# Optimization experiments

Hardware: AMD Instinct MI355X
Metric: run time of the kernel (lower is better)

The kernel has to match this reference:

```python
import jax, jax.numpy as jnp
import numpy as np

N = 25000      # nodes
E = 400000     # edges (before self-loops)
D = 64         # input node feature dim
H = 4          # attention heads
C = 64         # out channels per head (concat=False -> head mean)
L = 3          # stacked layers
NEG_SLOPE = 0.2
EPS = 1e-5


def setup_inputs() -> dict:
    key = jax.random.key(0)
    ks = jax.random.split(key, 8)
    s = 0.1
    return {
        "x": jax.random.normal(ks[0], (N, D), jnp.float32),
        "edge_index": jax.random.randint(ks[1], (2, E), 0, N, dtype=jnp.int64),
        "Wl": jax.random.normal(ks[2], (L, H * C, D), jnp.float32) * s,
        "bl": jnp.zeros((L, H * C), jnp.float32),
        "Wr": jax.random.normal(ks[3], (L, H * C, D), jnp.float32) * s,
        "br": jnp.zeros((L, H * C), jnp.float32),
        "att": jax.random.normal(ks[4], (L, H, C), jnp.float32) * s,
        "conv_bias": jnp.zeros((L, C), jnp.float32),
        "gn_weight": jnp.ones((L, C), jnp.float32),
        "gn_scale": jnp.ones((L, C), jnp.float32),   # GraphNorm mean_scale (alpha)
        "gn_bias": jnp.zeros((L, C), jnp.float32),
    }


def _gat_forward(x, src, dst, Wl, bl, Wr, br, att, conv_bias,
                 gn_weight, gn_scale, gn_bias):
    n = x.shape[0]
    for i in range(L):
        # GATv2Conv (edge_attr=None, concat=False): separate source/target projections
        xl = (x @ Wl[i].T + bl[i]).reshape(n, H, C)  # [N,H,C]
        xr = (x @ Wr[i].T + br[i]).reshape(n, H, C)
        # per-edge attention logits: att . leaky_relu(xl[j] + xr[i])
        e = jax.nn.leaky_relu(xl[src] + xr[dst], NEG_SLOPE)      # [E',H,C]
        logits = jnp.einsum('ehc,hc->eh', e, att[i])             # [E',H]
        # segment softmax over incoming edges of each target node
        m = jax.ops.segment_max(logits, dst, num_segments=n)     # [N,H]
        a = jnp.exp(logits - m[dst])
        denom = jax.ops.segment_sum(a, dst, num_segments=n)      # [N,H]
        alpha = a / denom[dst]                                   # [E',H]
        # weighted scatter-add of source messages, mean over heads
        agg = jax.ops.segment_sum(xl[src] * alpha[:, :, None], dst,
                                  num_segments=n)                # [N,H,C]
        h = agg.mean(axis=1) + conv_bias[i]                      # [N,C]
        # GraphNorm (single graph): x - alpha*mean, scale by rstd
        mu = h.mean(axis=0)
        hc = h - gn_scale[i] * mu
        var = jnp.mean(hc * hc, axis=0)
        x = hc * jax.lax.rsqrt(var + EPS) * gn_weight[i] + gn_bias[i]
        # Dropout p=0 at eval -> identity
    return x


def reference(x, edge_index, Wl, bl, Wr, br, att, conv_bias,
              gn_weight, gn_scale, gn_bias):
    n = x.shape[0]
    loop = jnp.arange(n, dtype=edge_index.dtype)
    # PyG GATv2Conv adds self-loops by default
    src = jnp.concatenate([edge_index[0], loop])
    dst = jnp.concatenate([edge_index[1], loop])
    return _gat_forward(x, src, dst, Wl, bl, Wr, br, att, conv_bias,
                        gn_weight, gn_scale, gn_bias)
```

## Files before the change

### kernel.cpp

```cpp
#include <hip/hip_runtime.h>
#include <hip/hip_fp16.h>
#include <math.h>

#define HC   256
#define DD   64
#define CC   64
#define NLAY 3

#define RCAP    64
#define RCAP_SH 6

typedef _Float16 h2 __attribute__((ext_vector_type(2)));
typedef _Float16 h4 __attribute__((ext_vector_type(4)));
typedef _Float16 h8 __attribute__((ext_vector_type(8)));
typedef float    f4 __attribute__((ext_vector_type(4)));
typedef float    f2 __attribute__((ext_vector_type(2)));

#define XSTR 72

__global__ __launch_bounds__(256) void zero_kernel(int* __restrict__ counts,
                                                   float* __restrict__ stats,
                                                   int n) {
    int i = blockIdx.x * 256 + threadIdx.x;
    if (i < n) counts[i] = 0;
    if (i < NLAY * 128) stats[i] = 0.f;
}

__global__ __launch_bounds__(256) void fill_kernel(const int* __restrict__ srcArr,
                                                   const int* __restrict__ dstArr,
                                                   int* __restrict__ counts,
                                                   int* __restrict__ csr_src,
                                                   int e, int n) {
    int i = blockIdx.x * 256 + threadIdx.x;
    if (i >= e + n) return;
    int s, d;
    if (i < e) { s = srcArr[i]; d = dstArr[i]; }
    else       { s = d = i - e; }
    int slot = atomicAdd(&counts[d], 1);
    if (slot < RCAP) csr_src[(d << RCAP_SH) + slot] = s;
}

__global__ __launch_bounds__(256) void proj_kernel(const float* __restrict__ x,
                                                   const float* __restrict__ Wl,
                                                   const float* __restrict__ bl,
                                                   const float* __restrict__ Wr,
                                                   const float* __restrict__ br,
                                                   __half* __restrict__ xl,
                                                   __half* __restrict__ xr, int n,
                                                   const float* __restrict__ stats,
                                                   const float* __restrict__ pgw,
                                                   const float* __restrict__ pgs,
                                                   const float* __restrict__ pgb) {
    __shared__ _Float16 xs[64 * XSTR];
    __shared__ _Float16 ws[256 * XSTR];
    __shared__ float nrm_a[64], nrm_b[64];
    const int t  = threadIdx.x;
    const int n0 = blockIdx.x * 64;
    const float* Wsel = blockIdx.y ? Wr : Wl;
    const float* bsel = blockIdx.y ? br : bl;
    __half*      osel = blockIdx.y ? xr : xl;

    if (t < 64) {
        float a = 1.f, b = 0.f;
        if (stats) {
            float inv_n = 1.0f / (float)n;
            float mu  = stats[t] * inv_n;
            float eh2 = stats[64 + t] * inv_n;
            float al  = pgs[t];
            float var = eh2 - 2.f * al * mu * mu + al * al * mu * mu;
            float rstd = rsqrtf(var + 1e-5f);
            a = pgw[t] * rstd;
            b = pgb[t] - al * mu * a;
        }
        nrm_a[t] = a; nrm_b[t] = b;
    }
    __syncthreads();

    {
        const float* xb = x + (size_t)n0 * DD;
        const int limit = (n - n0) * DD;
        #pragma unroll
        for (int it = 0; it < 4; ++it) {
            int f = (it * 256 + t) * 4;
            float4 v = make_float4(0.f, 0.f, 0.f, 0.f);
            if (f + 3 < limit) v = *(const float4*)(xb + f);
            else {
                float tmp[4] = {0.f, 0.f, 0.f, 0.f};
                for (int q = 0; q < 4; ++q) if (f + q < limit) tmp[q] = xb[f + q];
                v = make_float4(tmp[0], tmp[1], tmp[2], tmp[3]);
            }
            int d = f & 63;
            const float4 a4 = *(const float4*)&nrm_a[d];
            const float4 b4 = *(const float4*)&nrm_b[d];
            h4 hv;
            hv.x = (_Float16)fmaf(v.x, a4.x, b4.x);
            hv.y = (_Float16)fmaf(v.y, a4.y, b4.y);
            hv.z = (_Float16)fmaf(v.z, a4.z, b4.z);
            hv.w = (_Float16)fmaf(v.w, a4.w, b4.w);
            *(h4*)&xs[(f >> 6) * XSTR + d] = hv;
        }
    }
    {
        #pragma unroll
        for (int it = 0; it < 16; ++it) {
            int f = (it * 256 + t) * 4;
            float4 v = *(const float4*)(Wsel + f);
            h4 hv = { (_Float16)v.x, (_Float16)v.y, (_Float16)v.z, (_Float16)v.w };
            *(h4*)&ws[(f >> 6) * XSTR + (f & 63)] = hv;
        }
    }
    __syncthreads();

    const int w = t >> 6, lane = t & 63, m = lane & 15, q = lane >> 4;
    const _Float16* arow = xs + (w * 16 + m) * XSTR + q * 8;
    const h8 A0 = *(const h8*)arow;
    const h8 A1 = *(const h8*)(arow + 32);
    f4 acc[16];
    #pragma unroll
    for (int ct = 0; ct < 16; ++ct) {
        const _Float16* brow = ws + (ct * 16 + m) * XSTR + q * 8;
        const h8 B0 = *(const h8*)brow;
        const h8 B1 = *(const h8*)(brow + 32);
        f4 c = {0.f, 0.f, 0.f, 0.f};
        c = __builtin_amdgcn_mfma_f32_16x16x32_f16(A0, B0, c, 0, 0, 0);
        c = __builtin_amdgcn_mfma_f32_16x16x32_f16(A1, B1, c, 0, 0, 0);
        acc[ct] = c;
    }
    #pragma unroll
    for (int ct = 0; ct < 16; ++ct) {
        int ch = ct * 16 + m;
        float bv = bsel[ch];
        #pragma unroll
        for (int r = 0; r < 4; ++r) {
            int node = n0 + w * 16 + q * 4 + r;
            if (node < n)
                osel[(size_t)node * HC + ch] = __float2half(acc[ct][r] + bv);
        }
    }
}

__global__ __launch_bounds__(256) void attn_kernel(const __half* __restrict__ xl,
                                                   const __half* __restrict__ xr,
                                                   const float* __restrict__ att,
                                                   const float* __restrict__ conv_bias,
                                                   const int* __restrict__ counts,
                                                   const int* __restrict__ csr_src,
                                                   float* __restrict__ h_out, int n) {
    const int wave = threadIdx.x >> 6;
    const int l    = threadIdx.x & 63;
    const int v    = blockIdx.x * 4 + wave;
    if (v >= n) return;

    const int e2 = l >> 5;
    const int h  = (l >> 3) & 3;
    const int co = l & 7;
    const int choff = h * CC + co * 8;

    h2 xr2[4];
    *(uint4*)xr2 = *(const uint4*)(xr + (size_t)v * HC + choff);
    h2 at2[4];
    {
        const float* ap = att + choff;
        float4 a0 = *(const float4*)(ap);
        float4 a1 = *(const float4*)(ap + 4);
        at2[0] = (h2){(_Float16)a0.x, (_Float16)a0.y};
        at2[1] = (h2){(_Float16)a0.z, (_Float16)a0.w};
        at2[2] = (h2){(_Float16)a1.x, (_Float16)a1.y};
        at2[3] = (h2){(_Float16)a1.z, (_Float16)a1.w};
    }
    const _Float16 k02 = (_Float16)0.2f;

    const int rs = v << RCAP_SH;
    const int re = rs + counts[v];

    float s = 0.f;
    h2 acch[4];
    #pragma unroll
    for (int q = 0; q < 4; ++q) acch[q] = (h2){(_Float16)0.f, (_Float16)0.f};

    #define CLAMPI(i) (((i) < re) ? (i) : rs)

    uint4 r0 = *(const uint4*)(xl + (size_t)csr_src[CLAMPI(rs + e2)]     * HC + choff);
    uint4 r1 = *(const uint4*)(xl + (size_t)csr_src[CLAMPI(rs + 2 + e2)] * HC + choff);
    uint4 r2 = *(const uint4*)(xl + (size_t)csr_src[CLAMPI(rs + 4 + e2)] * HC + choff);
    int jnA = csr_src[CLAMPI(rs + 6 + e2)];
    int jnB = csr_src[CLAMPI(rs + 8 + e2)];
    int jnC = csr_src[CLAMPI(rs + 10 + e2)];

    #define STAGE(RBUF, JREG, VOFF, JOFF)                                 \
    {                                                                     \
        const uint4 cur = RBUF;                                           \
        RBUF = *(const uint4*)(xl + (size_t)JREG * HC + choff);           \
        JREG = csr_src[CLAMPI(k + JOFF + e2)];                            \
        const bool valid = (k + VOFF + e2) < re;                          \
        const h2* xh = (const h2*)&cur;                                   \
        h2 d2 = (h2){(_Float16)0.f, (_Float16)0.f};                      \
        _Pragma("unroll")                                                 \
        for (int q = 0; q < 4; ++q) {                                     \
            h2 tt = xh[q] + xr2[q];                                       \
            h2 lk = __builtin_elementwise_max(tt, tt * k02);              \
            d2 += lk * at2[q];                                            \
        }                                                                 \
        float p = (float)d2.x + (float)d2.y;                              \
        p += __shfl_xor(p, 1, 64);                                        \
        p += __shfl_xor(p, 2, 64);                                        \
        p += __shfl_xor(p, 4, 64);                                        \
        float pe = valid ? __expf(p) : 0.f;                               \
        s += pe;                                                          \
        const _Float16 peh = (_Float16)pe;                                \
        const h2 pe2 = (h2){peh, peh};                                    \
        _Pragma("unroll")                                                 \
        for (int q = 0; q < 4; ++q)                                       \
            acch[q] += pe2 * xh[q];                                       \
    }

    for (int k = rs; k < re; k += 6) {
        STAGE(r0, jnA, 0, 12)
        STAGE(r1, jnB, 2, 14)
        STAGE(r2, jnC, 4, 16)
    }
    #undef STAGE
    #undef CLAMPI

    s += __shfl_xor(s, 32, 64);
    const float inv = 1.f / s;
    float out8[8];
    #pragma unroll
    for (int q = 0; q < 8; ++q) {
        float av = (q & 1) ? (float)acch[q >> 1].y : (float)acch[q >> 1].x;
        float a = av + __shfl_xor(av, 32, 64);
        a *= inv;
        a += __shfl_xor(a, 8, 64);
        a += __shfl_xor(a, 16, 64);
        out8[q] = 0.25f * a;
    }
    if (l < 8) {
        const float4 cb0 = *(const float4*)(conv_bias + co * 8);
        const float4 cb1 = *(const float4*)(conv_bias + co * 8 + 4);
        float4 o0 = make_float4(out8[0] + cb0.x, out8[1] + cb0.y,
                                out8[2] + cb0.z, out8[3] + cb0.w);
        float4 o1 = make_float4(out8[4] + cb1.x, out8[5] + cb1.y,
                                out8[6] + cb1.z, out8[7] + cb1.w);
        float* op = h_out + (size_t)v * CC + co * 8;
        *(float4*)op       = o0;
        *(float4*)(op + 4) = o1;
    }
}

__global__ __launch_bounds__(256) void stats_kernel(const float* __restrict__ h,
                                                    float* __restrict__ stats, int n) {
    int t = threadIdx.x;
    int c = t & 63, r = t >> 6;
    float s = 0.f, s2 = 0.f;
    for (int node = blockIdx.x * 4 + r; node < n; node += gridDim.x * 4) {
        float v = h[node * CC + c];
        s += v; s2 += v * v;
    }
    __shared__ float l1[256], l2[256];
    l1[t] = s; l2[t] = s2;
    __syncthreads();
    if (t < 64) {
        s  = l1[t] + l1[64 + t] + l1[128 + t] + l1[192 + t];
        s2 = l2[t] + l2[64 + t] + l2[128 + t] + l2[192 + t];
        atomicAdd(&stats[c], s);
        atomicAdd(&stats[64 + c], s2);
    }
}

__global__ __launch_bounds__(256) void norm_kernel(const float* __restrict__ h,
                                                   const float* __restrict__ stats,
                                                   const float* __restrict__ gw,
                                                   const float* __restrict__ gs,
                                                   const float* __restrict__ gb,
                                                   float* __restrict__ out, int n) {
    __shared__ float na[64], nb[64];
    int t = threadIdx.x;
    if (t < 64) {
        float inv_n = 1.0f / (float)n;
        float mu  = stats[t] * inv_n;
        float eh2 = stats[64 + t] * inv_n;
        float a   = gs[t];
        float var = eh2 - 2.f * a * mu * mu + a * a * mu * mu;
        float rstd = rsqrtf(var + 1e-5f);
        na[t] = gw[t] * rstd;
        nb[t] = gb[t] - a * mu * gw[t] * rstd;
    }
    __syncthreads();
    int c = t & 63;
    float w = na[c], b = nb[c];
    int total = n * CC;
    for (int idx = blockIdx.x * 256 + t; idx < total; idx += gridDim.x * 256)
        out[idx] = fmaf(h[idx], w, b);
}

extern "C" void kernel_launch(void* const* d_in, const int* in_sizes, int n_in,
                              void* d_out, int out_size, void* d_ws, size_t ws_size,
                              hipStream_t stream) {
    const float* x0  = (const float*)d_in[0];
    const int*   ei  = (const int*)d_in[1];
    const float* Wl  = (const float*)d_in[2];
    const float* bl  = (const float*)d_in[3];
    const float* Wr  = (const float*)d_in[4];
    const float* br  = (const float*)d_in[5];
    const float* att = (const float*)d_in[6];
    const float* cb  = (const float*)d_in[7];
    const float* gw  = (const float*)d_in[8];
    const float* gs  = (const float*)d_in[9];
    const float* gb  = (const float*)d_in[10];

    const int n = in_sizes[0] / DD;
    const int e = in_sizes[1] / 2;
    const int* srcArr = ei;
    const int* dstArr = ei + e;

    char* w = (char*)d_ws;
    auto alloc = [&](size_t bytes) -> char* {
        char* p = w;
        w += (bytes + 255) & ~(size_t)255;
        return p;
    };
    __half* xl    = (__half*)alloc((size_t)n * HC * 2);
    __half* xr    = (__half*)alloc((size_t)n * HC * 2);
    float* hbuf   = (float*)alloc((size_t)n * CC * 4);
    int*   counts = (int*)  alloc((size_t)n * 4);
    int*   csr    = (int*)  alloc((size_t)n * RCAP * 4);
    float* stats  = (float*)alloc(NLAY * 128 * 4);

    const int tot = e + n;
    hipLaunchKernelGGL(zero_kernel,  dim3((n + 255) / 256),   dim3(256), 0, stream,
                       counts, stats, n);
    hipLaunchKernelGGL(fill_kernel,  dim3((tot + 255) / 256), dim3(256), 0, stream,
                       srcArr, dstArr, counts, csr, e, n);

    for (int L = 0; L < NLAY; ++L) {
        const float* xin = (L == 0) ? x0 : hbuf;
        const int Lp = (L == 0) ? 0 : L - 1;
        const float* st = (L == 0) ? nullptr : stats + (size_t)Lp * 128;
        hipLaunchKernelGGL(proj_kernel, dim3((n + 63) / 64, 2), dim3(256), 0, stream,
                           xin, Wl + (size_t)L * HC * DD, bl + L * HC,
                           Wr + (size_t)L * HC * DD, br + L * HC, xl, xr, n,
                           st, gw + Lp * CC, gs + Lp * CC, gb + Lp * CC);
        hipLaunchKernelGGL(attn_kernel, dim3((n + 3) / 4), dim3(256), 0, stream,
                           xl, xr, att + L * HC, cb + L * CC, counts, csr, hbuf, n);
        hipLaunchKernelGGL(stats_kernel, dim3(128), dim3(256), 0, stream,
                           hbuf, stats + (size_t)L * 128, n);
    }
    hipLaunchKernelGGL(norm_kernel, dim3(512), dim3(256), 0, stream,
                       hbuf, stats + (size_t)(NLAY - 1) * 128, gw + (NLAY - 1) * CC,
                       gs + (NLAY - 1) * CC, gb + (NLAY - 1) * CC,
                       (float*)d_out, n);
}
```

Before: 324.5 us.

## Compute both projections per block and stage outputs through LDS for coalesced stores

The projection kernel now handles both Wl and Wr in one block, so the normalized x tile is loaded and converted once instead of twice, and the grid drops its second dimension. Results are written to shared memory (reusing the weight buffer with a padded stride) and then stored to global memory as 16-byte rows instead of scattered 2-byte half stores. This adds several block barriers, serializes the two weight passes within a block, and halves the number of blocks.

```diff
diff --git a/kernel.cpp b/kernel.cpp
--- a/kernel.cpp
+++ b/kernel.cpp
@@ -17,6 +17,7 @@
 typedef float    f2 __attribute__((ext_vector_type(2)));
 
 #define XSTR 72
+#define OSTR 276
 
 __global__ __launch_bounds__(256) void zero_kernel(int* __restrict__ counts,
                                                    float* __restrict__ stats,
@@ -56,9 +57,6 @@
     __shared__ float nrm_a[64], nrm_b[64];
     const int t  = threadIdx.x;
     const int n0 = blockIdx.x * 64;
-    const float* Wsel = blockIdx.y ? Wr : Wl;
-    const float* bsel = blockIdx.y ? br : bl;
-    __half*      osel = blockIdx.y ? xr : xl;
 
     if (t < 64) {
         float a = 1.f, b = 0.f;
@@ -100,43 +98,81 @@
             *(h4*)&xs[(f >> 6) * XSTR + d] = hv;
         }
     }
+
+    const int w = t >> 6, lane = t & 63, m = lane & 15, q = lane >> 4;
+
+    h8 A0, A1;
+    f4 acc[16];
+
+    #define STAGE_W(Wsel)                                                     \
+    {                                                                         \
+        _Pragma("unroll")                                                     \
+        for (int it = 0; it < 16; ++it) {                                     \
+            int f = (it * 256 + t) * 4;                                       \
+            float4 v = *(const float4*)((Wsel) + f);                          \
+            h4 hv = { (_Float16)v.x, (_Float16)v.y, (_Float16)v.z,            \
+                      (_Float16)v.w };                                        \
+            *(h4*)&ws[(f >> 6) * XSTR + (f & 63)] = hv;                       \
+        }                                                                     \
+    }
+
+    #define MFMA_PASS()                                                       \
+    {                                                                         \
+        _Pragma("unroll")                                                     \
+        for (int ct = 0; ct < 16; ++ct) {                                     \
+            const _Float16* brow = ws + (ct * 16 + m) * XSTR + q * 8;         \
+            const h8 B0 = *(const h8*)brow;                                   \
+            const h8 B1 = *(const h8*)(brow + 32);                            \
+            f4 c = {0.f, 0.f, 0.f, 0.f};                                      \
+            c = __builtin_amdgcn_mfma_f32_16x16x32_f16(A0, B0, c, 0, 0, 0);   \
+            c = __builtin_amdgcn_mfma_f32_16x16x32_f16(A1, B1, c, 0, 0, 0);   \
+            acc[ct] = c;                                                      \
+        }                                                                     \
+    }
+
+    #define EPILOGUE(bsel, osel)                                              \
+    {                                                                         \
+        _Pragma("unroll")                                                     \
+        for (int ct = 0; ct < 16; ++ct) {                                     \
+            int ch = ct * 16 + m;                                             \
+            float bv = (bsel)[ch];                                            \
+            _Pragma("unroll")                                                 \
+            for (int r = 0; r < 4; ++r)                                       \
+                ws[(w * 16 + q * 4 + r) * OSTR + ch] =                        \
+                    (_Float16)(acc[ct][r] + bv);                              \
+        }                                                                     \
+        __syncthreads();                                                      \
+        _Pragma("unroll")                                                     \
+        for (int it = 0; it < 8; ++it) {                                      \
+            int f   = (it * 256 + t) * 8;                                     \
+            int row = f >> 8, ch = f & 255;                                   \
+            if (n0 + row < n)                                                 \
+                *(uint4*)((osel) + (size_t)(n0 + row) * HC + ch) =            \
+                    *(const uint4*)&ws[row * OSTR + ch];                      \
+        }                                                                     \
+    }
+
+    STAGE_W(Wl)
+    __syncthreads();
     {
-        #pragma unroll
-        for (int it = 0; it < 16; ++it) {
-            int f = (it * 256 + t) * 4;
-            float4 v = *(const float4*)(Wsel + f);
-            h4 hv = { (_Float16)v.x, (_Float16)v.y, (_Float16)v.z, (_Float16)v.w };
-            *(h4*)&ws[(f >> 6) * XSTR + (f & 63)] = hv;
-        }
-    }
-    __syncthreads();
-
-    const int w = t >> 6, lane = t & 63, m = lane & 15, q = lane >> 4;
-    const _Float16* arow = xs + (w * 16 + m) * XSTR + q * 8;
-    const h8 A0 = *(const h8*)arow;
-    const h8 A1 = *(const h8*)(arow + 32);
-    f4 acc[16];
-    #pragma unroll
-    for (int ct = 0; ct < 16; ++ct) {
-        const _Float16* brow = ws + (ct * 16 + m) * XSTR + q * 8;
-        const h8 B0 = *(const h8*)brow;
-        const h8 B1 = *(const h8*)(brow + 32);
-        f4 c = {0.f, 0.f, 0.f, 0.f};
-        c = __builtin_amdgcn_mfma_f32_16x16x32_f16(A0, B0, c, 0, 0, 0);
-        c = __builtin_amdgcn_mfma_f32_16x16x32_f16(A1, B1, c, 0, 0, 0);
-        acc[ct] = c;
-    }
-    #pragma unroll
-    for (int ct = 0; ct < 16; ++ct) {
-        int ch = ct * 16 + m;
-        float bv = bsel[ch];
-        #pragma unroll
-        for (int r = 0; r < 4; ++r) {
-            int node = n0 + w * 16 + q * 4 + r;
-            if (node < n)
-                osel[(size_t)node * HC + ch] = __float2half(acc[ct][r] + bv);
-        }
-    }
+        const _Float16* arow = xs + (w * 16 + m) * XSTR + q * 8;
+        A0 = *(const h8*)arow;
+        A1 = *(const h8*)(arow + 32);
+    }
+    MFMA_PASS()
+    __syncthreads();
+    EPILOGUE(bl, xl)
+    __syncthreads();
+
+    STAGE_W(Wr)
+    __syncthreads();
+    MFMA_PASS()
+    __syncthreads();
+    EPILOGUE(br, xr)
+
+    #undef STAGE_W
+    #undef MFMA_PASS
+    #undef EPILOGUE
 }
 
 __global__ __launch_bounds__(256) void attn_kernel(const __half* __restrict__ xl,
@@ -336,7 +372,7 @@
         const float* xin = (L == 0) ? x0 : hbuf;
         const int Lp = (L == 0) ? 0 : L - 1;
         const float* st = (L == 0) ? nullptr : stats + (size_t)Lp * 128;
-        hipLaunchKernelGGL(proj_kernel, dim3((n + 63) / 64, 2), dim3(256), 0, stream,
+        hipLaunchKernelGGL(proj_kernel, dim3((n + 63) / 64), dim3(256), 0, stream,
                            xin, Wl + (size_t)L * HC * DD, bl + L * HC,
                            Wr + (size_t)L * HC * DD, br + L * HC, xl, xr, n,
                            st, gw + Lp * CC, gs + Lp * CC, gb + Lp * CC);
```

Measured after the change: 301.2 us. -7.2%, faster.
